# Kernel tuning notes

Hardware: AMD Instinct MI355X
Metric: run time of the kernel (lower is better)

Reference implementation:

```python
import jax, jax.numpy as jnp
import numpy as np

EPS = 1e-08


def setup_inputs() -> dict:
    key = jax.random.key(0)
    k1, k2 = jax.random.split(key)
    query_features = jax.random.normal(k1, (64, 1024, 32, 32), dtype=jnp.float32)
    support_features = jax.random.normal(k2, (25, 1024, 32, 32), dtype=jnp.float32)
    return {"query_features": query_features, "support_features": support_features}


def reference(query_features, support_features):
    B, C, h, w = support_features.shape
    NQ = query_features.shape[0]
    # Covariance over channels: flatten support to (C, B*h*w), center, GEMM.
    support = jnp.transpose(support_features, (1, 0, 2, 3)).reshape(C, -1)
    centered = support - jnp.mean(support, axis=1, keepdims=True)
    N = B * h * w
    cov = (centered @ centered.T) / (N - 1 + EPS)  # (C, C)
    # Queries: (NQ, C, d), L2-normalize each channel row over spatial dim.
    q = query_features.reshape(NQ, C, -1)
    q = q / (jnp.linalg.norm(q, axis=2, keepdims=True) + EPS)
    # diag(q^T cov q) without materializing (d, d): cov@q then elementwise reduce over C.
    cq = jnp.einsum('cD,nDd->ncd', cov, q)  # (NQ, C, d)
    scores = jnp.mean(jnp.sum(q * cq, axis=1), axis=1)  # (NQ,)
    return scores
```

## Files before the change

kernel.cpp:

```cpp
#include <hip/hip_runtime.h>

#define NQ   64
#define CCH  1024
#define DSP  1024
#define NSUP 25600

typedef __attribute__((ext_vector_type(4))) float f32x4;
typedef __attribute__((ext_vector_type(8))) __bf16 bf16x8;

#define WAITVM(N) asm volatile("s_waitcnt vmcnt(" #N ")" ::: "memory")
#define WAITLGKM0() asm volatile("s_waitcnt lgkmcnt(0)" ::: "memory")
#define BAR() __builtin_amdgcn_s_barrier()
#define SCHED0() __builtin_amdgcn_sched_barrier(0)

__device__ inline unsigned short f2bf(float x) {
  unsigned u = __builtin_bit_cast(unsigned, x);
  u += 0x7fffu + ((u >> 16) & 1u);
  return (unsigned short)(u >> 16);
}

__global__ __launch_bounds__(256) void zero_kernel(float4* __restrict__ cov4,
                                                   float4* __restrict__ out4) {
  const int i = blockIdx.x * 256 + threadIdx.x;
  cov4[i] = make_float4(0.f, 0.f, 0.f, 0.f);
  if (i < 16) out4[i] = make_float4(0.f, 0.f, 0.f, 0.f);
}


__global__ __launch_bounds__(512) void mean_center_kernel(
    const float* __restrict__ sup, float* __restrict__ mean,
    unsigned short* __restrict__ Sb, int write_sb) {
  __shared__ float4 row[6400];
  __shared__ float red[512];
  const int c = blockIdx.x;
  const int tid = threadIdx.x;
  float s = 0.f;
  for (int qd = tid; qd < 6400; qd += 512) {
    const int b = qd >> 8, s4 = (qd & 255) << 2;
    const float4 v = *(const float4*)(sup + ((size_t)b * CCH + c) * DSP + s4);
    row[qd] = v;
    s += v.x + v.y + v.z + v.w;
  }
  red[tid] = s;
  __syncthreads();
  for (int st = 256; st > 0; st >>= 1) {
    if (tid < st) red[tid] += red[tid + st];
    __syncthreads();
  }
  const float m = red[0] * (1.0f / 25600.0f);
  if (tid == 0) mean[c] = m;
  if (write_sb) {
    for (int qd = tid; qd < 6400; qd += 512) {
      const float4 v = row[qd];
      const int b = qd >> 8, s4 = (qd & 255) << 2;
      ushort4 o;
      o.x = f2bf(v.x - m); o.y = f2bf(v.y - m);
      o.z = f2bf(v.z - m); o.w = f2bf(v.w - m);
      *(ushort4*)(Sb + (size_t)c * NSUP + b * DSP + s4) = o;
    }
  }
}

__global__ __launch_bounds__(256) void qnorm_kernel(
    const float* __restrict__ q, float* __restrict__ qfac,
    unsigned short* __restrict__ Qb, int write_qb) {
  const int row = blockIdx.x * 4 + (threadIdx.x >> 6);
  const int l = threadIdx.x & 63;
  const float4* src = (const float4*)(q + (size_t)row * DSP);
  float4 v[4];
  float ss = 0.f;
#pragma unroll
  for (int i = 0; i < 4; ++i) {
    v[i] = src[l + 64 * i];
    ss += v[i].x * v[i].x + v[i].y * v[i].y + v[i].z * v[i].z + v[i].w * v[i].w;
  }
#pragma unroll
  for (int off = 32; off > 0; off >>= 1) ss += __shfl_xor(ss, off);
  const float f = 1.0f / (sqrtf(ss) + 1e-8f);
  if (l == 0) qfac[row] = f;
  if (write_qb) {
#pragma unroll
    for (int i = 0; i < 4; ++i) {
      ushort4 o;
      o.x = f2bf(v[i].x * f); o.y = f2bf(v[i].y * f);
      o.z = f2bf(v[i].z * f); o.w = f2bf(v[i].w * f);
      *(ushort4*)(Qb + (size_t)row * DSP + (size_t)(l + 64 * i) * 4) = o;
    }
  }
}


__device__ inline void rd4(const unsigned short* base, int r0, int col, int lr, bf16x8 f[4]) {
#pragma unroll
  for (int i = 0; i < 4; ++i)
    f[i] = *(const bf16x8*)(const void*)(base + (r0 + i * 16 + lr) * 64 + col);
}
__device__ inline void mfma16(const bf16x8 a[4], const bf16x8 b[4], f32x4 (*acc)[4]) {
  __builtin_amdgcn_s_setprio(1);
#pragma unroll
  for (int i = 0; i < 4; ++i)
#pragma unroll
    for (int j = 0; j < 4; ++j)
      acc[i][j] = __builtin_amdgcn_mfma_f32_16x16x32_bf16(a[i], b[j], acc[i][j], 0, 0, 0);
  __builtin_amdgcn_s_setprio(0);
}


__device__ inline void stage256g(const unsigned short* __restrict__ src, int ld,
                                 int row0, int k0, unsigned short* lds_base) {
  const int tid = threadIdx.x;
  const int wid = tid >> 6;
#pragma unroll
  for (int it = 0; it < 4; ++it) {
    const int ci = it * 512 + tid;
    const int r = ci >> 3;
    const int kc = ((ci & 7) ^ (r & 7)) << 3;
    const unsigned short* g = src + (size_t)(row0 + r) * ld + k0 + kc;
    unsigned short* lb = lds_base + ((it * 512 + (wid << 6)) << 3);
    __builtin_amdgcn_global_load_lds((const __attribute__((address_space(1))) void*)g,
                                     (__attribute__((address_space(3))) void*)lb,
                                     16, 0, 0);
  }
}

template <int NT>
__device__ inline void loop256(const unsigned short* __restrict__ src, int ld,
                               int rowA, int rowB, int k0, bool diag,
                               unsigned short* lds,
                               int wm, int wn, int lr, int kg, int sw,
                               f32x4 (*acc)[4]) {
  stage256g(src, ld, rowA, k0, lds);
  if (!diag) stage256g(src, ld, rowB, k0, lds + 16384);
  stage256g(src, ld, rowA, k0 + 64, lds + 32768);
  if (!diag) stage256g(src, ld, rowB, k0 + 64, lds + 32768 + 16384);

  for (int t = 0; t < NT; ++t) {
    const int cb = (t & 1) << 15;
    if (t < NT - 1) { if (diag) { WAITVM(4); } else { WAITVM(8); } }
    else { WAITVM(0); }
    BAR(); SCHED0();
    const unsigned short* A = lds + cb + wm * 8192;
    const unsigned short* B = lds + cb + (diag ? 0 : 16384) + (wn >> 1) * 8192;
    const int brow = (wn & 1) * 64;
    bf16x8 a[4], b[4];
    {
      const int col = kg ^ sw;
      rd4(B, brow, col, lr, b);
      rd4(A, 0, col, lr, a);
      mfma16(a, b, &acc[0]);
      rd4(A, 64, col, lr, a);
      mfma16(a, b, &acc[4]);
    }
    {
      const int col = (32 + kg) ^ sw;
      rd4(B, brow, col, lr, b);
      rd4(A, 0, col, lr, a);
      mfma16(a, b, &acc[0]);
      rd4(A, 64, col, lr, a);
      WAITLGKM0();
      BAR(); SCHED0();
      if (t + 2 < NT) {
        stage256g(src, ld, rowA, k0 + (t + 2) * 64, lds + cb);
        if (!diag) stage256g(src, ld, rowB, k0 + (t + 2) * 64, lds + cb + 16384);
      }
      mfma16(a, b, &acc[4]);
    }
  }
}

__device__ inline void decode_pair4(int p, int& ti, int& tj) {
  int rem = p; ti = 0;
  while (rem >= 4 - ti) { rem -= 4 - ti; ++ti; }
  tj = ti + rem;
}

__global__ __launch_bounds__(512, 2) void cov256_kernel(
    const unsigned short* __restrict__ Sb, float* __restrict__ cov) {
  __shared__ unsigned short lds[65536];
  const int wg = blockIdx.x;
  const int g = (wg & 7) * 32 + (wg >> 3);
  if (g >= 250) return;
  const int ks = g / 10;
  int ti, tj; decode_pair4(g % 10, ti, tj);
  const bool diag = (ti == tj);
  const int tid = threadIdx.x, l = tid & 63, wid = tid >> 6;
  const int wm = wid >> 2, wn = wid & 3;
  const int lr = l & 15, kg = (l >> 4) * 8;
  const int sw = (lr & 7) << 3;

  f32x4 acc[8][4];
#pragma unroll
  for (int i = 0; i < 8; ++i)
#pragma unroll
    for (int j = 0; j < 4; ++j) acc[i][j] = 0.f;

  loop256<16>(Sb, NSUP, ti * 256, tj * 256, ks * 1024, diag, lds,
              wm, wn, lr, kg, sw, acc);

  const float scale = 1.0f / (25599.0f + 1e-8f);
  const int rbase = ti * 256 + wm * 128 + (l >> 4) * 4;
  const int cbase = tj * 256 + wn * 64 + (l & 15);
#pragma unroll
  for (int i = 0; i < 8; ++i)
#pragma unroll
    for (int j = 0; j < 4; ++j)
#pragma unroll
      for (int r = 0; r < 4; ++r)
        atomicAdd(&cov[(size_t)(rbase + i * 16 + r) * CCH + cbase + j * 16],
                  acc[i][j][r] * scale);
}

__global__ __launch_bounds__(512, 2) void gram256_kernel(
    const unsigned short* __restrict__ Qb, const float* __restrict__ cov,
    float* __restrict__ out) {
  __shared__ unsigned short lds[65536];
  const int wg = blockIdx.x;
  const int xcd = wg & 7, slot = wg >> 3;
  const int n = xcd * 8 + slot / 20;
  const int sub = slot % 20;
  const int kh = sub & 1;
  int ti, tj; decode_pair4(sub >> 1, ti, tj);
  const bool diag = (ti == tj);
  const int tid = threadIdx.x, l = tid & 63, wid = tid >> 6;
  const int wm = wid >> 2, wn = wid & 3;
  const int lr = l & 15, kg = (l >> 4) * 8;
  const int sw = (lr & 7) << 3;
  const unsigned short* Qn = Qb + (size_t)n * CCH * DSP;

  f32x4 acc[8][4];
#pragma unroll
  for (int i = 0; i < 8; ++i)
#pragma unroll
    for (int j = 0; j < 4; ++j) acc[i][j] = 0.f;

  loop256<8>(Qn, DSP, ti * 256, tj * 256, kh * 512, diag, lds,
             wm, wn, lr, kg, sw, acc);

  float s = 0.f;
  const int rbase = ti * 256 + wm * 128 + (l >> 4) * 4;
  const int cbase = tj * 256 + wn * 64 + (l & 15);
#pragma unroll
  for (int i = 0; i < 8; ++i)
#pragma unroll
    for (int j = 0; j < 4; ++j)
#pragma unroll
      for (int r = 0; r < 4; ++r)
        s += acc[i][j][r] * cov[(size_t)(rbase + i * 16 + r) * CCH + cbase + j * 16];
  if (!diag) s *= 2.0f;
  s *= (1.0f / 1024.0f);
#pragma unroll
  for (int off = 32; off > 0; off >>= 1) s += __shfl_xor(s, off);
  if (l == 0) atomicAdd(&out[n], s);
}

__device__ inline void mfma16s(const bf16x8 a[4], const bf16x8 b[4], f32x4 acc[4][4]) {
#pragma unroll
  for (int i = 0; i < 4; ++i)
#pragma unroll
    for (int j = 0; j < 4; ++j)
      acc[i][j] = __builtin_amdgcn_mfma_f32_16x16x32_bf16(a[i], b[j], acc[i][j], 0, 0, 0);
}

__device__ inline void stage_sup_f32(const float* __restrict__ sup,
                                     const float* __restrict__ mean,
                                     int row0, int k0, unsigned short* lds) {
  const int tid = threadIdx.x;
#pragma unroll
  for (int it = 0; it < 4; ++it) {
    const int ci = it * 256 + tid;
    const int r = ci >> 3, kc = (ci & 7) << 3;
    const int c = row0 + r;
    const int k = k0 + kc;
    const int b = k >> 10, sp = k & 1023;
    const float4* gp = (const float4*)(sup + ((size_t)b * CCH + c) * DSP + sp);
    const float4 v0 = gp[0], v1 = gp[1];
    const float m = mean[c];
    union { unsigned short h[8]; int4 q; } pk;
    pk.h[0] = f2bf(v0.x - m); pk.h[1] = f2bf(v0.y - m);
    pk.h[2] = f2bf(v0.z - m); pk.h[3] = f2bf(v0.w - m);
    pk.h[4] = f2bf(v1.x - m); pk.h[5] = f2bf(v1.y - m);
    pk.h[6] = f2bf(v1.z - m); pk.h[7] = f2bf(v1.w - m);
    *(int4*)(lds + (size_t)(r * 8 + ((ci & 7) ^ (r & 7))) * 8) = pk.q;
  }
}
__device__ inline void stage_q_f32(const float* __restrict__ qn,
                                   const float* __restrict__ qfacn,
                                   int row0, int k0, unsigned short* lds) {
  const int tid = threadIdx.x;
#pragma unroll
  for (int it = 0; it < 4; ++it) {
    const int ci = it * 256 + tid;
    const int r = ci >> 3, kc = (ci & 7) << 3;
    const int c = row0 + r;
    const float4* gp = (const float4*)(qn + (size_t)c * DSP + k0 + kc);
    const float4 v0 = gp[0], v1 = gp[1];
    const float f = qfacn[c];
    union { unsigned short h[8]; int4 q; } pk;
    pk.h[0] = f2bf(v0.x * f); pk.h[1] = f2bf(v0.y * f);
    pk.h[2] = f2bf(v0.z * f); pk.h[3] = f2bf(v0.w * f);
    pk.h[4] = f2bf(v1.x * f); pk.h[5] = f2bf(v1.y * f);
    pk.h[6] = f2bf(v1.z * f); pk.h[7] = f2bf(v1.w * f);
    *(int4*)(lds + (size_t)(r * 8 + ((ci & 7) ^ (r & 7))) * 8) = pk.q;
  }
}
__device__ inline void compute_step(const unsigned short* lA, const unsigned short* lB,
                                    int wr, int wc, int lr, int kg, f32x4 acc[4][4]) {
  const int sc = (lr & 7) << 3;
#pragma unroll
  for (int kk = 0; kk < 64; kk += 32) {
    const int col = (kk + kg) ^ sc;
    bf16x8 a[4], b[4];
    rd4(lA, wr, col, lr, a);
    rd4(lB, wc, col, lr, b);
    mfma16s(a, b, acc);
  }
}
__device__ inline void decode_tile8(int t, int& ti, int& tj) {
  int rem = t; ti = 0;
  while (rem >= 8 - ti) { rem -= 8 - ti; ++ti; }
  tj = ti + rem;
}

__global__ __launch_bounds__(256) void cov_kernel_f32(
    const float* __restrict__ sup, const float* __restrict__ mean,
    float* __restrict__ cov) {
  __shared__ unsigned short clds[32768];
  const int wg = blockIdx.x;
  const int ks = wg & 7;
  int ti, tj; decode_tile8(wg >> 3, ti, tj);
  const bool diag = (ti == tj);
  const int tid = threadIdx.x, l = tid & 63, w = tid >> 6;
  const int wr = (w >> 1) * 64, wc = (w & 1) * 64, lr = l & 15, kg = (l >> 4) * 8;
  f32x4 acc[4][4];
#pragma unroll
  for (int i = 0; i < 4; ++i)
#pragma unroll
    for (int j = 0; j < 4; ++j) acc[i][j] = 0.f;

  const int kbase = ks * (NSUP / 8);
  stage_sup_f32(sup, mean, ti * 128, kbase, clds);
  if (!diag) stage_sup_f32(sup, mean, tj * 128, kbase, clds + 8192);
  __syncthreads();
  for (int kt = 0; kt < 50; ++kt) {
    const int cb = (kt & 1) * 16384;
    const int nb = cb ^ 16384;
    if (kt + 1 < 50) {
      const int k1 = kbase + (kt + 1) * 64;
      stage_sup_f32(sup, mean, ti * 128, k1, clds + nb);
      if (!diag) stage_sup_f32(sup, mean, tj * 128, k1, clds + nb + 8192);
    }
    compute_step(clds + cb, diag ? clds + cb : clds + cb + 8192, wr, wc, lr, kg, acc);
    __syncthreads();
  }
  const float scale = 1.0f / (25599.0f + 1e-8f);
  const int rbase = ti * 128 + wr + (l >> 4) * 4;
  const int cbase = tj * 128 + wc + (l & 15);
#pragma unroll
  for (int i = 0; i < 4; ++i)
#pragma unroll
    for (int j = 0; j < 4; ++j)
#pragma unroll
      for (int r = 0; r < 4; ++r)
        atomicAdd(&cov[(size_t)(rbase + i * 16 + r) * CCH + cbase + j * 16],
                  acc[i][j][r] * scale);
}

__global__ __launch_bounds__(256) void gram_kernel_f32(
    const float* __restrict__ q, const float* __restrict__ qfac,
    const float* __restrict__ cov, float* __restrict__ out) {
  __shared__ unsigned short lA[2][128 * 64];
  __shared__ unsigned short lB[2][128 * 64];
  const int wg = blockIdx.x;
  const int xcd = wg & 7, slot = wg >> 3;
  const int n = xcd * 8 + slot / 36;
  int ti, tj; decode_tile8(slot % 36, ti, tj);
  const bool diag = (ti == tj);
  const int tid = threadIdx.x, l = tid & 63, w = tid >> 6;
  const int wr = (w >> 1) * 64, wc = (w & 1) * 64, lr = l & 15, kg = (l >> 4) * 8;
  f32x4 acc[4][4];
#pragma unroll
  for (int i = 0; i < 4; ++i)
#pragma unroll
    for (int j = 0; j < 4; ++j) acc[i][j] = 0.f;

  const float* qn = q + (size_t)n * CCH * DSP;
  const float* qfacn = qfac + (size_t)n * CCH;

  stage_q_f32(qn, qfacn, ti * 128, 0, lA[0]);
  if (!diag) stage_q_f32(qn, qfacn, tj * 128, 0, lB[0]);
  __syncthreads();
  int cur = 0;
  for (int kt = 0; kt < 16; ++kt) {
    if (kt + 1 < 16) {
      const int k1 = (kt + 1) * 64;
      stage_q_f32(qn, qfacn, ti * 128, k1, lA[cur ^ 1]);
      if (!diag) stage_q_f32(qn, qfacn, tj * 128, k1, lB[cur ^ 1]);
    }
    compute_step(lA[cur], diag ? lA[cur] : lB[cur], wr, wc, lr, kg, acc);
    __syncthreads();
    cur ^= 1;
  }

  float s = 0.f;
  const int rbase = ti * 128 + wr + (l >> 4) * 4;
  const int cbase = tj * 128 + wc + (l & 15);
#pragma unroll
  for (int i = 0; i < 4; ++i)
#pragma unroll
    for (int j = 0; j < 4; ++j)
#pragma unroll
      for (int r = 0; r < 4; ++r)
        s += acc[i][j][r] * cov[(size_t)(rbase + i * 16 + r) * CCH + cbase + j * 16];
  if (!diag) s *= 2.0f;
  s *= (1.0f / 1024.0f);
#pragma unroll
  for (int off = 32; off > 0; off >>= 1) s += __shfl_xor(s, off);
  if (l == 0) atomicAdd(&out[n], s);
}

extern "C" void kernel_launch(void* const* d_in, const int* in_sizes, int n_in,
                              void* d_out, int out_size, void* d_ws, size_t ws_size,
                              hipStream_t stream) {
  const float* q = (const float*)d_in[0];
  const float* sup = (const float*)d_in[1];
  float* out = (float*)d_out;

  char* ws = (char*)d_ws;
  float* mean = (float*)ws;
  float* qfac = (float*)(ws + (4 << 10));
  float* cov  = (float*)(ws + (4 << 10) + (256 << 10));
  unsigned short* Sb = (unsigned short*)(ws + (4 << 10) + (256 << 10) + (4 << 20));
  unsigned short* Qb = Sb + (size_t)CCH * NSUP;
  const size_t need_fat = (size_t)(4 << 10) + (256 << 10) + (4 << 20) +
                          (size_t)CCH * NSUP * 2 + (size_t)NQ * CCH * DSP * 2;
  const bool fat = ws_size >= need_fat;

  zero_kernel<<<1024, 256, 0, stream>>>((float4*)cov, (float4*)out);

  mean_center_kernel<<<CCH, 512, 0, stream>>>(sup, mean, Sb, fat ? 1 : 0);
  qnorm_kernel<<<NQ * CCH / 4, 256, 0, stream>>>(q, qfac, Qb, fat ? 1 : 0);

  if (fat) {
    cov256_kernel<<<dim3(256), 512, 0, stream>>>(Sb, cov);
    gram256_kernel<<<dim3(1280), 512, 0, stream>>>(Qb, cov, out);
  } else {
    cov_kernel_f32<<<dim3(288), 256, 0, stream>>>(sup, mean, cov);
    gram_kernel_f32<<<dim3(8 * 8 * 36), 256, 0, stream>>>(q, qfac, cov, out);
  }
}
```

Measured before the change: 301.6 us.

## Retile covariance GEMM to 128 tiles and drop gram K-split

The covariance kernel now uses 128x128 upper-triangle tiles (36 tile pairs × 8 K-splits, 256 threads) with a double-buffered global-to-LDS pipeline, replacing the previous 256-tile, 25-way K-split kernel. Off-diagonal tiles that fall inside a 256-wide diagonal block are mirrored with extra atomics, so the gram kernel can still read the lower half of its diagonal blocks. The gram kernel no longer splits K in half: each block processes the full 1024 depth, which halves the grid and the atomics into the output. The trade-off is less parallelism and a possibly uneven final wave in gram, and lower data reuse per block in cov.

```diff
diff --git a/kernel.cpp b/kernel.cpp
--- a/kernel.cpp
+++ b/kernel.cpp
@@ -4,6 +4,7 @@
 #define CCH  1024
 #define DSP  1024
 #define NSUP 25600
+#define NK_COV 50
 
 typedef __attribute__((ext_vector_type(4))) float f32x4;
 typedef __attribute__((ext_vector_type(8))) __bf16 bf16x8;
@@ -105,6 +106,22 @@
   __builtin_amdgcn_s_setprio(0);
 }
 
+__device__ inline void stage_glds(const unsigned short* __restrict__ src, int ld,
+                                  int row0, int k0, unsigned short* lds) {
+  const int tid = threadIdx.x;
+  const int w = tid >> 6;
+#pragma unroll
+  for (int it = 0; it < 4; ++it) {
+    const int ci = it * 256 + tid;
+    const int r = ci >> 3;
+    const int kc = ((ci & 7) ^ (r & 7)) << 3;
+    const unsigned short* g = src + (size_t)(row0 + r) * ld + k0 + kc;
+    unsigned short* lb = lds + ((it * 256 + w * 64) << 3);
+    __builtin_amdgcn_global_load_lds((const __attribute__((address_space(1))) void*)g,
+                                     (__attribute__((address_space(3))) void*)lb,
+                                     16, 0, 0);
+  }
+}
 
 __device__ inline void stage256g(const unsigned short* __restrict__ src, int ld,
                                  int row0, int k0, unsigned short* lds_base) {
@@ -168,46 +185,83 @@
   }
 }
 
+__device__ inline void decode_tile8(int t, int& ti, int& tj) {
+  int rem = t; ti = 0;
+  while (rem >= 8 - ti) { rem -= 8 - ti; ++ti; }
+  tj = ti + rem;
+}
 __device__ inline void decode_pair4(int p, int& ti, int& tj) {
   int rem = p; ti = 0;
   while (rem >= 4 - ti) { rem -= 4 - ti; ++ti; }
   tj = ti + rem;
 }
 
-__global__ __launch_bounds__(512, 2) void cov256_kernel(
+__global__ __launch_bounds__(256) void cov128_kernel(
     const unsigned short* __restrict__ Sb, float* __restrict__ cov) {
-  __shared__ unsigned short lds[65536];
+  __shared__ unsigned short clds[32768];
   const int wg = blockIdx.x;
-  const int g = (wg & 7) * 32 + (wg >> 3);
-  if (g >= 250) return;
-  const int ks = g / 10;
-  int ti, tj; decode_pair4(g % 10, ti, tj);
+  const int ks = wg & 7;
+  int ti, tj; decode_tile8(wg >> 3, ti, tj);
   const bool diag = (ti == tj);
-  const int tid = threadIdx.x, l = tid & 63, wid = tid >> 6;
-  const int wm = wid >> 2, wn = wid & 3;
-  const int lr = l & 15, kg = (l >> 4) * 8;
+  const bool mirror = (!(ti & 1)) && (tj == ti + 1);
+  const int tid = threadIdx.x, l = tid & 63, w = tid >> 6;
+  const int wr = (w >> 1) * 64, wc = (w & 1) * 64, lr = l & 15, kg = (l >> 4) * 8;
   const int sw = (lr & 7) << 3;
-
-  f32x4 acc[8][4];
-#pragma unroll
-  for (int i = 0; i < 8; ++i)
+  f32x4 acc[4][4];
+#pragma unroll
+  for (int i = 0; i < 4; ++i)
 #pragma unroll
     for (int j = 0; j < 4; ++j) acc[i][j] = 0.f;
 
-  loop256<16>(Sb, NSUP, ti * 256, tj * 256, ks * 1024, diag, lds,
-              wm, wn, lr, kg, sw, acc);
+  const int kbase = ks * (NSUP / 8);
+
+  stage_glds(Sb, NSUP, ti * 128, kbase, clds);
+  if (!diag) stage_glds(Sb, NSUP, tj * 128, kbase, clds + 8192);
+  stage_glds(Sb, NSUP, ti * 128, kbase + 64, clds + 16384);
+  if (!diag) stage_glds(Sb, NSUP, tj * 128, kbase + 64, clds + 16384 + 8192);
+  for (int t = 0; t < NK_COV; ++t) {
+    const int cb = (t & 1) * 16384;
+    if (t < NK_COV - 1) { if (diag) { WAITVM(4); } else { WAITVM(8); } }
+    else { WAITVM(0); }
+    BAR(); SCHED0();
+    const unsigned short* A = clds + cb;
+    const unsigned short* B = diag ? A : A + 8192;
+    bf16x8 a[4], b[4];
+    {
+      const int col = kg ^ sw;
+      rd4(A, wr, col, lr, a);
+      rd4(B, wc, col, lr, b);
+      mfma16(a, b, (f32x4(*)[4])acc);
+    }
+    {
+      const int col = (32 + kg) ^ sw;
+      rd4(A, wr, col, lr, a);
+      rd4(B, wc, col, lr, b);
+      WAITLGKM0();
+      BAR(); SCHED0();
+      if (t + 2 < NK_COV) {
+        const int k2 = kbase + (t + 2) * 64;
+        stage_glds(Sb, NSUP, ti * 128, k2, clds + cb);
+        if (!diag) stage_glds(Sb, NSUP, tj * 128, k2, clds + cb + 8192);
+      }
+      mfma16(a, b, (f32x4(*)[4])acc);
+    }
+  }
 
   const float scale = 1.0f / (25599.0f + 1e-8f);
-  const int rbase = ti * 256 + wm * 128 + (l >> 4) * 4;
-  const int cbase = tj * 256 + wn * 64 + (l & 15);
-#pragma unroll
-  for (int i = 0; i < 8; ++i)
-#pragma unroll
-    for (int j = 0; j < 4; ++j)
-#pragma unroll
-      for (int r = 0; r < 4; ++r)
-        atomicAdd(&cov[(size_t)(rbase + i * 16 + r) * CCH + cbase + j * 16],
-                  acc[i][j][r] * scale);
+  const int rbase = ti * 128 + wr + (l >> 4) * 4;
+  const int cbase = tj * 128 + wc + (l & 15);
+#pragma unroll
+  for (int i = 0; i < 4; ++i)
+#pragma unroll
+    for (int j = 0; j < 4; ++j)
+#pragma unroll
+      for (int r = 0; r < 4; ++r) {
+        const float v = acc[i][j][r] * scale;
+        atomicAdd(&cov[(size_t)(rbase + i * 16 + r) * CCH + cbase + j * 16], v);
+        if (mirror)
+          atomicAdd(&cov[(size_t)(cbase + j * 16) * CCH + rbase + i * 16 + r], v);
+      }
 }
 
 __global__ __launch_bounds__(512, 2) void gram256_kernel(
@@ -216,10 +270,8 @@
   __shared__ unsigned short lds[65536];
   const int wg = blockIdx.x;
   const int xcd = wg & 7, slot = wg >> 3;
-  const int n = xcd * 8 + slot / 20;
-  const int sub = slot % 20;
-  const int kh = sub & 1;
-  int ti, tj; decode_pair4(sub >> 1, ti, tj);
+  const int n = xcd * 8 + slot / 10;
+  int ti, tj; decode_pair4(slot % 10, ti, tj);
   const bool diag = (ti == tj);
   const int tid = threadIdx.x, l = tid & 63, wid = tid >> 6;
   const int wm = wid >> 2, wn = wid & 3;
@@ -233,8 +285,8 @@
 #pragma unroll
     for (int j = 0; j < 4; ++j) acc[i][j] = 0.f;
 
-  loop256<8>(Qn, DSP, ti * 256, tj * 256, kh * 512, diag, lds,
-             wm, wn, lr, kg, sw, acc);
+  loop256<16>(Qn, DSP, ti * 256, tj * 256, 0, diag, lds,
+              wm, wn, lr, kg, sw, acc);
 
   float s = 0.f;
   const int rbase = ti * 256 + wm * 128 + (l >> 4) * 4;
@@ -315,11 +367,6 @@
     mfma16s(a, b, acc);
   }
 }
-__device__ inline void decode_tile8(int t, int& ti, int& tj) {
-  int rem = t; ti = 0;
-  while (rem >= 8 - ti) { rem -= 8 - ti; ++ti; }
-  tj = ti + rem;
-}
 
 __global__ __launch_bounds__(256) void cov_kernel_f32(
     const float* __restrict__ sup, const float* __restrict__ mean,
@@ -441,8 +488,8 @@
   qnorm_kernel<<<NQ * CCH / 4, 256, 0, stream>>>(q, qfac, Qb, fat ? 1 : 0);
 
   if (fat) {
-    cov256_kernel<<<dim3(256), 512, 0, stream>>>(Sb, cov);
-    gram256_kernel<<<dim3(1280), 512, 0, stream>>>(Qb, cov, out);
+    cov128_kernel<<<dim3(288), 256, 0, stream>>>(Sb, cov);
+    gram256_kernel<<<dim3(640), 512, 0, stream>>>(Qb, cov, out);
   } else {
     cov_kernel_f32<<<dim3(288), 256, 0, stream>>>(sup, mean, cov);
     gram_kernel_f32<<<dim3(8 * 8 * 36), 256, 0, stream>>>(q, qfac, cov, out);
```

After: 279.3 us. -7.4%, faster.
